# Kernel tuning notes

Hardware: AMD Instinct MI355X
Metric: run time of the kernel (lower is better)

## Reference

```python
import jax, jax.numpy as jnp
import numpy as np

B, S, D, H, HD = 1, 4096, 512, 8, 64
FF = 2048
ROT = 32          # rotary dim (RotaryEmbedding(dim=32))
THETA = 10000.0
EPS = 1e-5


def setup_inputs() -> dict:
    key = jax.random.key(0)
    ks = jax.random.split(key, 10)
    s = 0.02
    return {
        "x": jax.random.normal(ks[0], (B, S, D), jnp.float32),
        "gammas": jnp.ones((2,), jnp.float32),
        "betas": jnp.zeros((2,), jnp.float32),
        "wq": jax.random.normal(ks[1], (D, D), jnp.float32) * s,
        "wk": jax.random.normal(ks[2], (D, D), jnp.float32) * s,
        "wv": jax.random.normal(ks[3], (D, D), jnp.float32) * s,
        "wo": jax.random.normal(ks[4], (D, D), jnp.float32) * s,
        "bo": jnp.zeros((D,), jnp.float32),
        "w1": jax.random.normal(ks[5], (D, FF), jnp.float32) * s,
        "b1": jnp.zeros((FF,), jnp.float32),
        "w2": jax.random.normal(ks[6], (FF, D), jnp.float32) * s,
        "b2": jnp.zeros((D,), jnp.float32),
        "mask": jax.random.randint(ks[7], (B, 1, 1, S), 0, 2, jnp.int32),
    }


def _ln(x):  # LayerNorm, no affine (elementwise_affine=False)
    m = x.mean(-1, keepdims=True)
    v = ((x - m) ** 2).mean(-1, keepdims=True)
    return (x - m) / jnp.sqrt(v + EPS)


def _rope_tables(seq_len, dtype):
    inv_freq = 1.0 / (THETA ** (jnp.arange(0, ROT, 2, dtype=jnp.float32) / ROT))
    freqs = jnp.arange(seq_len, dtype=jnp.float32)[:, None] * inv_freq[None, :]  # (S, ROT/2)
    freqs = jnp.repeat(freqs, 2, axis=-1)  # interleaved: f0,f0,f1,f1,... (S, ROT)
    return jnp.cos(freqs).astype(dtype), jnp.sin(freqs).astype(dtype)


def _apply_rope(t, cos, sin):
    # t: (B,H,S,HD); rotate first ROT dims with interleaved pairs (lucidrains)
    tr, tp = t[..., :ROT], t[..., ROT:]
    x1, x2 = tr[..., 0::2], tr[..., 1::2]
    rot = jnp.stack((-x2, x1), axis=-1).reshape(tr.shape)
    return jnp.concatenate([tr * cos + rot * sin, tp], axis=-1)


def reference(x, gammas, betas, wq, wk, wv, wo, bo, w1, b1, w2, b2, mask):
    # --- attention block ---
    res = x
    h = _ln(x)
    h = gammas[0] * h + betas[0]  # FiLM
    q = (h @ wq).reshape(B, S, H, HD).transpose(0, 2, 1, 3)
    k = (h @ wk).reshape(B, S, H, HD).transpose(0, 2, 1, 3)
    v = (h @ wv).reshape(B, S, H, HD).transpose(0, 2, 1, 3)
    cos, sin = _rope_tables(S, x.dtype)
    q = _apply_rope(q, cos, sin)
    k = _apply_rope(k, cos, sin)
    score = jnp.einsum("bhqd,bhkd->bhqk", q, k) / jnp.sqrt(jnp.asarray(HD, x.dtype))
    score = jnp.where(mask == 0, jnp.asarray(-1e9, x.dtype), score)
    attn = jax.nn.softmax(score, axis=-1)
    out = jnp.einsum("bhqk,bhkd->bhqd", attn, v)
    out = out.transpose(0, 2, 1, 3).reshape(B, S, D)
    x = res + (out @ wo + bo)
    # --- FFN block ---
    res = x
    h = _ln(x)
    h = gammas[1] * h + betas[1]
    h = jax.nn.gelu(h @ w1 + b1, approximate=False) @ w2 + b2
    return res + h
```

## Files before the change

kernel.cpp:

```cpp
#include <hip/hip_runtime.h>
#include <math.h>

constexpr int SEQ  = 4096;
constexpr int DIM  = 512;
constexpr int NH   = 8;
constexpr int HDIM = 64;
constexpr int FFD  = 2048;
constexpr int KSPLIT = 3;

typedef unsigned short u16;
typedef __attribute__((ext_vector_type(8))) short bf16x8;
typedef __attribute__((ext_vector_type(4))) float f32x4;
typedef __attribute__((ext_vector_type(8))) unsigned short u16x8;

#define LOG2E      1.4426950408889634f
#define QSCALE     (0.125f * LOG2E)
#define MASK_OFF   (-1.4427e9f)

static __device__ __forceinline__ u16 f2bf(float x) {
    union { float f; unsigned int u; } v; v.f = x;
    unsigned int r = v.u + 0x7fff + ((v.u >> 16) & 1);
    return (u16)(r >> 16);
}
static __device__ __forceinline__ float bf2f(u16 h) {
    union { unsigned int u; float f; } v; v.u = ((unsigned int)h) << 16;
    return v.f;
}
static __device__ __forceinline__ unsigned int cvtpk(float lo, float hi) {
    unsigned int r;
    asm volatile("v_cvt_pk_bf16_f32 %0, %1, %2" : "=v"(r) : "v"(lo), "v"(hi));
    return r;
}
static __device__ __forceinline__ float exp2f_fast(float x) {
    float r; asm volatile("v_exp_f32 %0, %1" : "=v"(r) : "v"(x)); return r;
}
static __device__ __forceinline__ void gload_lds16(const void* g, void* l) {
    __builtin_amdgcn_global_load_lds(
        (const __attribute__((address_space(1))) unsigned int*)g,
        (__attribute__((address_space(3))) unsigned int*)l, 16, 0, 0);
}

__global__ void prep_kernel(const float* __restrict__ x, u16* __restrict__ h1,
                            const float* __restrict__ gammas, const float* __restrict__ betas,
                            const float* __restrict__ wq, const float* __restrict__ wk,
                            const float* __restrict__ wv, const float* __restrict__ wo,
                            const float* __restrict__ w1, const float* __restrict__ w2,
                            u16* __restrict__ wqkvT, u16* __restrict__ woT,
                            u16* __restrict__ w1T, u16* __restrict__ w2T,
                            const int* __restrict__ mask, float* __restrict__ maskc,
                            int* __restrict__ invidx, int* __restrict__ nkp,
                            float* __restrict__ ct, float* __restrict__ st) {
    __shared__ float smem[1056];
    int b = blockIdx.x;
    int t = threadIdx.x;
    if (b < SEQ / 4) {
        int wv_ = t >> 6, lane = t & 63;
        int row = b * 4 + wv_;
        const float* xr = x + (size_t)row * DIM + lane * 8;
        float4 a0 = *(const float4*)xr;
        float4 a1 = *(const float4*)(xr + 4);
        float f[8] = {a0.x, a0.y, a0.z, a0.w, a1.x, a1.y, a1.z, a1.w};
        float s = 0.f, qs = 0.f;
#pragma unroll
        for (int i = 0; i < 8; i++) { s += f[i]; qs += f[i] * f[i]; }
#pragma unroll
        for (int o = 1; o < 64; o <<= 1) {
            s  += __shfl_xor(s, o, 64);
            qs += __shfl_xor(qs, o, 64);
        }
        float mean = s / DIM;
        float var  = qs / DIM - mean * mean;
        float rstd = rsqrtf(var + 1e-5f);
        float g = gammas[0], be = betas[0];
        u16x8 res;
#pragma unroll
        for (int i = 0; i < 8; i += 2) {
            unsigned int pk = cvtpk(g * ((f[i] - mean) * rstd) + be,
                                    g * ((f[i + 1] - mean) * rstd) + be);
            res[i]     = (u16)(pk & 0xffff);
            res[i + 1] = (u16)(pk >> 16);
        }
        *(u16x8*)(h1 + (size_t)row * DIM + lane * 8) = res;
        return;
    }
    b -= SEQ / 4;
    if (b < 1) {
        __shared__ int cnt[256];
        int base = t * 16;
        int loc[16]; int c = 0;
#pragma unroll
        for (int i = 0; i < 16; i++) { loc[i] = mask[base + i]; c += (loc[i] != 0); }
        cnt[t] = c;
        __syncthreads();
        for (int o = 1; o < 256; o <<= 1) {
            int v = (t >= o) ? cnt[t - o] : 0;
            __syncthreads();
            cnt[t] += v;
            __syncthreads();
        }
        int pos = cnt[t] - c;
        int total = cnt[255];
#pragma unroll
        for (int i = 0; i < 16; i++)
            invidx[base + i] = loc[i] ? pos++ : -1;
#pragma unroll
        for (int i = 0; i < 16; i++)
            maskc[base + i] = (base + i < total) ? 0.0f : MASK_OFF;
        if (t == 0) *nkp = total;
        return;
    }
    b -= 1;
    if (b < 256) {
        int idx = b * 256 + t;
        int s = idx >> 4, i = idx & 15;
        float invf = expf(-(float)i * (9.2103403719761836f / 16.0f));
        float freq = (float)s * invf;
        ct[idx] = cosf(freq);
        st[idx] = sinf(freq);
        return;
    }
    b -= 256;
    const float* src; u16* dst; int K, N; float scale = 1.f;
    if (b < 256)       { src = wq; dst = wqkvT;            K = 512;  N = 512; scale = QSCALE; }
    else if (b < 512)  { src = wk; dst = wqkvT + 512*512;  K = 512;  N = 512; b -= 256; }
    else if (b < 768)  { src = wv; dst = wqkvT + 1024*512; K = 512;  N = 512; b -= 512; }
    else if (b < 1024) { src = wo; dst = woT;              K = 512;  N = 512; b -= 768; }
    else if (b < 2048) { src = w1; dst = w1T;              K = 512;  N = 2048; b -= 1024; }
    else               { src = w2; dst = w2T;              K = 2048; N = 512;  b -= 2048; }
    float (*tile)[33] = (float(*)[33])smem;
    int tiles_x = N / 32;
    int n0 = (b % tiles_x) * 32, k0 = (b / tiles_x) * 32;
    int tx = t & 31, ty = t >> 5;
#pragma unroll
    for (int i = 0; i < 4; i++) {
        int kk = ty + i * 8;
        tile[kk][tx] = src[(size_t)(k0 + kk) * N + n0 + tx];
    }
    __syncthreads();
#pragma unroll
    for (int i = 0; i < 4; i++) {
        int nn = ty + i * 8;
        dst[(size_t)(n0 + nn) * K + k0 + tx] = f2bf(scale * tile[tx][nn]);
    }
}

__global__ void ln_bf16_kernel(const u16* __restrict__ x, u16* __restrict__ out,
                               const float* __restrict__ gammas, const float* __restrict__ betas,
                               int gi) {
    int t = threadIdx.x;
    int wv_ = t >> 6, lane = t & 63;
    int row = blockIdx.x * 4 + wv_;
    u16x8 v = *(const u16x8*)(x + (size_t)row * DIM + lane * 8);
    float f[8];
    float s = 0.f, qs = 0.f;
#pragma unroll
    for (int i = 0; i < 8; i++) { f[i] = bf2f(v[i]); s += f[i]; qs += f[i] * f[i]; }
#pragma unroll
    for (int o = 1; o < 64; o <<= 1) {
        s  += __shfl_xor(s, o, 64);
        qs += __shfl_xor(qs, o, 64);
    }
    float mean = s / DIM;
    float var  = qs / DIM - mean * mean;
    float rstd = rsqrtf(var + 1e-5f);
    float g = gammas[gi], be = betas[gi];
    u16x8 res;
#pragma unroll
    for (int i = 0; i < 8; i += 2) {
        unsigned int pk = cvtpk(g * ((f[i] - mean) * rstd) + be,
                                g * ((f[i + 1] - mean) * rstd) + be);
        res[i]     = (u16)(pk & 0xffff);
        res[i + 1] = (u16)(pk >> 16);
    }
    *(u16x8*)(out + (size_t)row * DIM + lane * 8) = res;
}

constexpr int FLAG_BF16 = 1, FLAG_GELU = 2, FLAG_SPLIT = 4, FLAG_ROPE = 8, FLAG_RESID_BF16 = 16;

template<int MF>
__global__ __launch_bounds__(256) void gemm_bf16(
    const u16* __restrict__ A, const u16* __restrict__ WT,
    const float* __restrict__ bias, const void* __restrict__ resid,
    void* __restrict__ Cq, int M, int N, int K, int flags)
{
    constexpr int BM = MF * 64;
    __shared__ __align__(16) u16 At[2][BM * 128];
    __shared__ __align__(16) u16 Bt[2][64 * 128];
    const int t = threadIdx.x, lane = t & 63, w = t >> 6;
    const int n0 = blockIdx.x * 64, m0 = blockIdx.y * BM;
    const int l15 = lane & 15, l4 = lane >> 4;

    f32x4 acc[MF][4];
#pragma unroll
    for (int m = 0; m < MF; m++)
#pragma unroll
        for (int n = 0; n < 4; n++) acc[m][n] = (f32x4){0.f, 0.f, 0.f, 0.f};

    auto stage = [&](int buf, int k0) {
#pragma unroll
        for (int i = 0; i < MF * 4; i++) {
            int c = (w * MF * 4 + i) * 64 + lane;
            int r = c >> 4, jj = (c & 15) ^ (r & 7);
            gload_lds16(A + (size_t)(m0 + r) * K + k0 + jj * 8,
                        (char*)At[buf] + (w * MF * 4 + i) * 1024);
        }
#pragma unroll
        for (int i = 0; i < 4; i++) {
            int c = (w * 4 + i) * 64 + lane;
            int r = c >> 4, jj = (c & 15) ^ (r & 7);
            gload_lds16(WT + (size_t)(n0 + r) * K + k0 + jj * 8,
                        (char*)Bt[buf] + (w * 4 + i) * 1024);
        }
    };

    const int NT = K / 128;
    stage(0, 0);
    for (int ti = 0; ti < NT; ti++) {
        const int cur = ti & 1;
        asm volatile("s_waitcnt vmcnt(0)" ::: "memory");
        __syncthreads();
        if (ti + 1 < NT) stage(cur ^ 1, (ti + 1) * 128);
        __builtin_amdgcn_s_setprio(1);
#pragma unroll
        for (int kk = 0; kk < 4; kk++) {
            bf16x8 af[MF], bfr[4];
#pragma unroll
            for (int m = 0; m < MF; m++) {
                int row = w * MF * 16 + m * 16 + l15;
                af[m] = *(bf16x8*)((char*)At[cur] + row * 256 +
                                   ((kk * 64 + l4 * 16) ^ ((row & 7) << 4)));
            }
#pragma unroll
            for (int n = 0; n < 4; n++) {
                int row = n * 16 + l15;
                bfr[n] = *(bf16x8*)((char*)Bt[cur] + row * 256 +
                                    ((kk * 64 + l4 * 16) ^ ((row & 7) << 4)));
            }
#pragma unroll
            for (int m = 0; m < MF; m++)
#pragma unroll
                for (int n = 0; n < 4; n++)
                    acc[m][n] = __builtin_amdgcn_mfma_f32_16x16x32_bf16(
                        af[m], bfr[n], acc[m][n], 0, 0, 0);
        }
        __builtin_amdgcn_s_setprio(0);
    }

#pragma unroll
    for (int m = 0; m < MF; m++)
#pragma unroll
        for (int rr = 0; rr < 4; rr++) {
            int row = m0 + w * MF * 16 + m * 16 + l4 * 4 + rr;
#pragma unroll
            for (int n = 0; n < 4; n++) {
                int colg = n0 + n * 16 + l15;
                float cv = acc[m][n][rr];
                if (bias) cv += bias[colg];
                if (flags & FLAG_GELU) cv = 0.5f * cv * (1.0f + erff(cv * 0.70710678118f));
                if (resid) {
                    if (flags & FLAG_RESID_BF16)
                        cv += bf2f(((const u16*)resid)[(size_t)row * N + colg]);
                    else
                        cv += ((const float*)resid)[(size_t)row * N + colg];
                }
                if (flags & FLAG_BF16) {
                    ((u16*)Cq)[(size_t)row * N + colg] = f2bf(cv);
                } else {
                    ((float*)Cq)[(size_t)row * N + colg] = cv;
                }
            }
        }
}

__global__ __launch_bounds__(256) void gemm128(
    const u16* __restrict__ A, const u16* __restrict__ WT,
    const float* __restrict__ bias,
    void* __restrict__ Cq, void* __restrict__ Ck, void* __restrict__ Cv,
    const float* __restrict__ ct, const float* __restrict__ st,
    const int* __restrict__ invidx,
    int M, int N, int K, int flags)
{
    __shared__ __align__(16) u16 At[2][128 * 64];
    __shared__ __align__(16) u16 Bt[2][128 * 64];
    const int t = threadIdx.x, lane = t & 63, w = t >> 6;
    const int wm = w >> 1, wn = w & 1;
    const int n0 = blockIdx.x * 128, m0 = blockIdx.y * 128;
    const int l15 = lane & 15, l4 = lane >> 4;

    f32x4 acc[4][4];
#pragma unroll
    for (int m = 0; m < 4; m++)
#pragma unroll
        for (int n = 0; n < 4; n++) acc[m][n] = (f32x4){0.f, 0.f, 0.f, 0.f};

    auto stage = [&](int buf, int k0) {
#pragma unroll
        for (int i = 0; i < 4; i++) {
            int c = (w * 4 + i) * 64 + lane;
            int r = c >> 3, j = (c & 7) ^ (r & 7);
            gload_lds16(A + (size_t)(m0 + r) * K + k0 + j * 8,
                        (char*)At[buf] + (w * 4 + i) * 1024);
            gload_lds16(WT + (size_t)(n0 + r) * K + k0 + j * 8,
                        (char*)Bt[buf] + (w * 4 + i) * 1024);
        }
    };

    const int NT = K / 64;
    stage(0, 0);
    for (int ti = 0; ti < NT; ti++) {
        const int cur = ti & 1;
        asm volatile("s_waitcnt vmcnt(0)" ::: "memory");
        __syncthreads();
        if (ti + 1 < NT) stage(cur ^ 1, (ti + 1) * 64);
        __builtin_amdgcn_s_setprio(1);
#pragma unroll
        for (int kk = 0; kk < 2; kk++) {
            bf16x8 af[4], bfr[4];
#pragma unroll
            for (int m = 0; m < 4; m++) {
                int row = wm * 64 + m * 16 + l15;
                af[m] = *(bf16x8*)((char*)At[cur] + row * 128 +
                                   ((kk * 64 + l4 * 16) ^ ((row & 7) << 4)));
            }
#pragma unroll
            for (int n = 0; n < 4; n++) {
                int row = wn * 64 + n * 16 + l15;
                bfr[n] = *(bf16x8*)((char*)Bt[cur] + row * 128 +
                                    ((kk * 64 + l4 * 16) ^ ((row & 7) << 4)));
            }
#pragma unroll
            for (int m = 0; m < 4; m++)
#pragma unroll
                for (int n = 0; n < 4; n++)
                    acc[m][n] = __builtin_amdgcn_mfma_f32_16x16x32_bf16(
                        af[m], bfr[n], acc[m][n], 0, 0, 0);
        }
        __builtin_amdgcn_s_setprio(0);
    }

    const int which = (n0 + wn * 64) >> 9;
#pragma unroll
    for (int m = 0; m < 4; m++)
#pragma unroll
        for (int rr = 0; rr < 4; rr++) {
            int row = m0 + wm * 64 + m * 16 + l4 * 4 + rr;
            int orow = row;
            if ((flags & FLAG_SPLIT) && which > 0) orow = invidx[row];
#pragma unroll
            for (int n = 0; n < 4; n++) {
                int colg = n0 + wn * 64 + n * 16 + l15;
                float cv = acc[m][n][rr];
                if (bias) cv += bias[colg];
                if ((flags & FLAG_ROPE) && which < 2 && n < 2) {
                    float partner = __shfl_xor(cv, 1, 64);
                    int i = (n * 16 + l15) >> 1;
                    float cc = ct[row * 16 + i], ss = st[row * 16 + i];
                    cv = (l15 & 1) ? (cv * cc + partner * ss) : (cv * cc - partner * ss);
                }
                if (flags & FLAG_GELU) cv = 0.5f * cv * (1.0f + erff(cv * 0.70710678118f));
                if (flags & FLAG_SPLIT) {
                    if (orow >= 0) {
                        u16* dst = which == 0 ? (u16*)Cq : which == 1 ? (u16*)Ck : (u16*)Cv;
                        dst[(size_t)orow * 512 + (colg & 511)] = f2bf(cv);
                    }
                } else {
                    ((u16*)Cq)[(size_t)row * N + colg] = f2bf(cv);
                }
            }
        }
}

__global__ void transpose_c(const u16* __restrict__ vc, const int* __restrict__ nkp,
                            u16* __restrict__ vTc) {
    int nk = *nkp;
    int s0 = blockIdx.x * 64;
    if (s0 >= ((nk + 63) & ~63)) return;
    __shared__ __align__(16) u16 tile[64][80];
    int h = blockIdx.y;
    int t = threadIdx.x;
#pragma unroll
    for (int p = 0; p < 2; p++) {
        int c = p * 256 + t;
        int r = c >> 3, j = c & 7;
        u16x8 vv = {};
        if (s0 + r < nk)
            vv = *(const u16x8*)(vc + (size_t)(s0 + r) * DIM + h * HDIM + j * 8);
        *(u16x8*)&tile[r][j * 8] = vv;
    }
    __syncthreads();
#pragma unroll
    for (int p = 0; p < 2; p++) {
        int c = p * 256 + t;
        int d = c >> 3, j = c & 7;
        u16x8 vv;
#pragma unroll
        for (int i = 0; i < 8; i++) vv[i] = tile[j * 8 + i][d];
        *(u16x8*)(vTc + ((size_t)h * HDIM + d) * SEQ + s0 + j * 8) = vv;
    }
}

__global__ __launch_bounds__(256, 3) void fattn_kernel(
    const u16* __restrict__ q, const u16* __restrict__ k,
    const u16* __restrict__ vT, const float* __restrict__ maskc,
    const int* __restrict__ nkp,
    u16* __restrict__ Opart, float* __restrict__ lpart)
{
    __shared__ __align__(16) u16 k_s[2][64 * 64];
    __shared__ __align__(16) u16 vt_s[2][64 * 64];
    __shared__ __align__(16) u16 p_s[4][32 * 64];

    const int t = threadIdx.x;
    const int lane = t & 63;
    const int w = t >> 6;
    const int h = blockIdx.x;
    const int q0 = blockIdx.y * 128;
    const int split = blockIdx.z;
    const int nk = *nkp;
    const int ntiles = (nk + 63) >> 6;
    const int tstart = (split * ntiles) / 3;
    const int tend   = ((split + 1) * ntiles) / 3;
    const int l15 = lane & 15, g = lane >> 4;

    bf16x8 qf[2][2];
#pragma unroll
    for (int qh = 0; qh < 2; qh++) {
        const u16* qrow = q + (size_t)(q0 + w * 32 + qh * 16 + l15) * DIM + h * HDIM;
        qf[qh][0] = *(const bf16x8*)(qrow + g * 8);
        qf[qh][1] = *(const bf16x8*)(qrow + g * 8 + 32);
    }

    const bf16x8 ones = (bf16x8){16256, 16256, 16256, 16256, 16256, 16256, 16256, 16256};

    f32x4 O[2][4];
    f32x4 lacc[2];
#pragma unroll
    for (int qh = 0; qh < 2; qh++) {
#pragma unroll
        for (int dt = 0; dt < 4; dt++) O[qh][dt] = (f32x4){0.f, 0.f, 0.f, 0.f};
        lacc[qh] = (f32x4){0.f, 0.f, 0.f, 0.f};
    }

    char* pbase = (char*)p_s[w];
    const int psw = (l15 & 7) << 4;

    auto stage = [&](int buf, int kb2) {
#pragma unroll
        for (int i = 0; i < 2; i++) {
            int c = (w * 2 + i) * 64 + lane;
            int r = c >> 3, j = (c & 7) ^ (r & 7);
            gload_lds16(k + (size_t)(kb2 + r) * DIM + h * HDIM + j * 8,
                        (char*)k_s + buf * 8192 + (w * 2 + i) * 1024);
            gload_lds16(vT + ((size_t)h * HDIM + r) * SEQ + kb2 + j * 8,
                        (char*)vt_s + buf * 8192 + (w * 2 + i) * 1024);
        }
    };

    if (tstart < tend) stage(0, tstart * 64);
    for (int ti = tstart; ti < tend; ti++) {
        const int cur = (ti - tstart) & 1;
        const int kb = ti * 64;
        asm volatile("s_waitcnt vmcnt(0)" ::: "memory");
        __syncthreads();
        if (ti + 1 < tend) stage(cur ^ 1, kb + 64);

        char* kcur = (char*)k_s + cur * 8192;
        char* vcur = (char*)vt_s + cur * 8192;

        f32x4 sacc[2][4];
        __builtin_amdgcn_s_setprio(1);
#pragma unroll
        for (int kt = 0; kt < 4; kt++) {
            int key = kt * 16 + l15;
            int ksw = (key & 7) << 4;
            char* kbase = kcur + key * 128;
            bf16x8 a0 = *(bf16x8*)(kbase + ((g * 16)      ^ ksw));
            bf16x8 a1 = *(bf16x8*)(kbase + ((g * 16 + 64) ^ ksw));
#pragma unroll
            for (int qh = 0; qh < 2; qh++) {
                f32x4 z = (f32x4){0.f, 0.f, 0.f, 0.f};
                z = __builtin_amdgcn_mfma_f32_16x16x32_bf16(a0, qf[qh][0], z, 0, 0, 0);
                z = __builtin_amdgcn_mfma_f32_16x16x32_bf16(a1, qf[qh][1], z, 0, 0, 0);
                sacc[qh][kt] = z;
            }
        }
        __builtin_amdgcn_s_setprio(0);

        const bool haspad = (ti == ntiles - 1);
        if (!haspad) {
#pragma unroll
            for (int qh = 0; qh < 2; qh++)
#pragma unroll
                for (int kt = 0; kt < 4; kt++) {
                    float p0 = exp2f_fast(sacc[qh][kt][0]);
                    float p1 = exp2f_fast(sacc[qh][kt][1]);
                    float p2 = exp2f_fast(sacc[qh][kt][2]);
                    float p3 = exp2f_fast(sacc[qh][kt][3]);
                    uint2 pk;
                    pk.x = cvtpk(p0, p1);
                    pk.y = cvtpk(p2, p3);
                    int colb = (kt * 16 + g * 4) * 2;
                    *(uint2*)(pbase + (qh * 16 + l15) * 128 + (colb ^ psw)) = pk;
                }
        } else {
            float4 mf4[4];
#pragma unroll
            for (int kt = 0; kt < 4; kt++)
                mf4[kt] = *(const float4*)(maskc + kb + kt * 16 + g * 4);
#pragma unroll
            for (int qh = 0; qh < 2; qh++)
#pragma unroll
                for (int kt = 0; kt < 4; kt++) {
                    float p0 = exp2f_fast(sacc[qh][kt][0] + mf4[kt].x);
                    float p1 = exp2f_fast(sacc[qh][kt][1] + mf4[kt].y);
                    float p2 = exp2f_fast(sacc[qh][kt][2] + mf4[kt].z);
                    float p3 = exp2f_fast(sacc[qh][kt][3] + mf4[kt].w);
                    uint2 pk;
                    pk.x = cvtpk(p0, p1);
                    pk.y = cvtpk(p2, p3);
                    int colb = (kt * 16 + g * 4) * 2;
                    *(uint2*)(pbase + (qh * 16 + l15) * 128 + (colb ^ psw)) = pk;
                }
        }

        __builtin_amdgcn_s_setprio(1);
#pragma unroll
        for (int h2 = 0; h2 < 2; h2++) {
            bf16x8 pb[2];
#pragma unroll
            for (int qh = 0; qh < 2; qh++)
                pb[qh] = *(bf16x8*)(pbase + (qh * 16 + l15) * 128 +
                                    (((h2 * 4 + g) * 16) ^ psw));
#pragma unroll
            for (int dt = 0; dt < 4; dt++) {
                int d = dt * 16 + l15;
                bf16x8 va = *(bf16x8*)(vcur + d * 128 +
                                       (((h2 * 4 + g) * 16) ^ ((d & 7) << 4)));
#pragma unroll
                for (int qh = 0; qh < 2; qh++)
                    O[qh][dt] = __builtin_amdgcn_mfma_f32_16x16x32_bf16(
                        va, pb[qh], O[qh][dt], 0, 0, 0);
            }
#pragma unroll
            for (int qh = 0; qh < 2; qh++)
                lacc[qh] = __builtin_amdgcn_mfma_f32_16x16x32_bf16(
                    ones, pb[qh], lacc[qh], 0, 0, 0);
        }
        __builtin_amdgcn_s_setprio(0);
    }

#pragma unroll
    for (int qh = 0; qh < 2; qh++) {
        float lrun = lacc[qh][0];
        int row = q0 + w * 32 + qh * 16 + l15;
        u16* orow = Opart + (size_t)split * SEQ * DIM + (size_t)row * DIM + h * HDIM;
#pragma unroll
        for (int dt = 0; dt < 4; dt++)
#pragma unroll
            for (int r = 0; r < 4; r += 2) {
                unsigned int pk = cvtpk(O[qh][dt][r], O[qh][dt][r + 1]);
                *(unsigned int*)(orow + dt * 16 + 4 * g + r) = pk;
            }
        if (g == 0)
            lpart[((size_t)split * NH + h) * SEQ + row] = lrun;
    }
}

__global__ void attn_combine(const u16* __restrict__ Opart, const float* __restrict__ lpart,
                             u16* __restrict__ out) {
    int t = threadIdx.x;
    int row = blockIdx.x * 4 + (t >> 6);
    int col = (t & 63) * 8;
    int h = col >> 6;
    float l = lpart[(size_t)h * SEQ + row]
            + lpart[((size_t)NH + h) * SEQ + row]
            + lpart[((size_t)2 * NH + h) * SEQ + row];
    float inv = 1.0f / l;
    const size_t SD = (size_t)SEQ * DIM;
    const u16* base = Opart + (size_t)row * DIM + col;
    u16x8 ua = *(const u16x8*)(base);
    u16x8 ub = *(const u16x8*)(base + SD);
    u16x8 uc = *(const u16x8*)(base + 2 * SD);
    u16x8 res;
#pragma unroll
    for (int j = 0; j < 8; j += 2) {
        float o0 = bf2f(ua[j])     + bf2f(ub[j])     + bf2f(uc[j]);
        float o1 = bf2f(ua[j + 1]) + bf2f(ub[j + 1]) + bf2f(uc[j + 1]);
        unsigned int pk = cvtpk(o0 * inv, o1 * inv);
        res[j]     = (u16)(pk & 0xffff);
        res[j + 1] = (u16)(pk >> 16);
    }
    *(u16x8*)(out + (size_t)row * DIM + col) = res;
}

extern "C" void kernel_launch(void* const* d_in, const int* in_sizes, int n_in,
                              void* d_out, int out_size, void* d_ws, size_t ws_size,
                              hipStream_t stream) {
    const float* x      = (const float*)d_in[0];
    const float* gammas = (const float*)d_in[1];
    const float* betas  = (const float*)d_in[2];
    const float* wq     = (const float*)d_in[3];
    const float* wk     = (const float*)d_in[4];
    const float* wv     = (const float*)d_in[5];
    const float* wo     = (const float*)d_in[6];
    const float* bo     = (const float*)d_in[7];
    const float* w1     = (const float*)d_in[8];
    const float* b1     = (const float*)d_in[9];
    const float* w2     = (const float*)d_in[10];
    const float* b2     = (const float*)d_in[11];
    const int*   mask   = (const int*)d_in[12];
    float* out = (float*)d_out;

    char* wsb = (char*)d_ws;
    u16*   h1b   = (u16*)(wsb + 0);
    u16*   kc    = (u16*)(wsb + (4ull  << 20));
    u16*   vc    = (u16*)(wsb + (8ull  << 20));
    u16*   vTc   = (u16*)(wsb + (12ull << 20));
    u16*   qb    = (u16*)(wsb + (16ull << 20));
    u16*   Opart = (u16*)(wsb + (20ull << 20));
    u16*   x2b   = (u16*)(wsb + (20ull << 20));
    u16*   wqkvT = (u16*)(wsb + (32ull << 20));
    u16*   woT   = wqkvT + 1536 * 512;
    u16*   w1T   = woT   + 512 * 512;
    u16*   w2T   = w1T   + 2048 * 512;
    float* maskc = (float*)(wsb + (38ull << 20));
    int*   invidx= (int*)(wsb + (38ull << 20) + (64 << 10));
    int*   nkp   = (int*)(wsb + (38ull << 20) + (128 << 10));
    float* ct    = (float*)(wsb + (39ull << 20));
    float* st    = ct + 65536;
    float* lpart = (float*)(wsb + (40ull << 20));
    u16*   f1b   = h1b;
    u16*   h2b   = qb;
    u16*   attnb = h1b;

    prep_kernel<<<SEQ / 4 + 1 + 256 + 3072, 256, 0, stream>>>(
        x, h1b, gammas, betas, wq, wk, wv, wo, w1, w2,
        wqkvT, woT, w1T, w2T, mask, maskc, invidx, nkp, ct, st);
    gemm128<<<dim3(1536 / 128, SEQ / 128), 256, 0, stream>>>(
        h1b, wqkvT, nullptr, qb, kc, vc, ct, st, invidx,
        SEQ, 1536, DIM, FLAG_SPLIT | FLAG_BF16 | FLAG_ROPE);
    transpose_c<<<dim3(SEQ / 64, NH), 256, 0, stream>>>(vc, nkp, vTc);
    fattn_kernel<<<dim3(NH, SEQ / 128, KSPLIT), 256, 0, stream>>>(
        qb, kc, vTc, maskc, nkp, Opart, lpart);
    attn_combine<<<SEQ / 4, 256, 0, stream>>>(Opart, lpart, attnb);
    gemm_bf16<1><<<dim3(DIM / 64, SEQ / 64), 256, 0, stream>>>(
        attnb, woT, bo, (const void*)x, x2b, SEQ, DIM, DIM, FLAG_BF16);
    ln_bf16_kernel<<<SEQ / 4, 256, 0, stream>>>(x2b, h2b, gammas, betas, 1);
    gemm128<<<dim3(FFD / 128, SEQ / 128), 256, 0, stream>>>(
        h2b, w1T, b1, f1b, nullptr, nullptr, nullptr, nullptr, nullptr,
        SEQ, FFD, DIM, FLAG_BF16 | FLAG_GELU);
    gemm_bf16<1><<<dim3(DIM / 64, SEQ / 64), 256, 0, stream>>>(
        f1b, w2T, b2, (const void*)x2b, out, SEQ, DIM, FFD, FLAG_RESID_BF16);
}
```

Measured before the change: 149.4 us.

## Fuse split-K attention combine into flash-attention kernel via last-block atomic counter

Removes the separate attn_combine launch. Each flash-attention block now takes a per-(head, query-tile) atomic ticket after a threadfence, and the last of the three splits reads the partial outputs and row sums and writes the normalized bf16 attention output. The counters are zeroed in the existing prep kernel. This saves a kernel launch and the gap between kernels, at the cost of extra fences, an atomic per block, and serialized combine work inside the tail blocks.

New measurement: 267.7 us. +79.1%, slower.

```diff
diff --git a/kernel.cpp b/kernel.cpp
--- a/kernel.cpp
+++ b/kernel.cpp
@@ -49,6 +49,7 @@
                             u16* __restrict__ w1T, u16* __restrict__ w2T,
                             const int* __restrict__ mask, float* __restrict__ maskc,
                             int* __restrict__ invidx, int* __restrict__ nkp,
+                            int* __restrict__ ccnt,
                             float* __restrict__ ct, float* __restrict__ st) {
     __shared__ float smem[1056];
     int b = blockIdx.x;
@@ -86,6 +87,7 @@
     b -= SEQ / 4;
     if (b < 1) {
         __shared__ int cnt[256];
+        ccnt[t] = 0;
         int base = t * 16;
         int loc[16]; int c = 0;
 #pragma unroll
@@ -403,7 +405,8 @@
     const u16* __restrict__ q, const u16* __restrict__ k,
     const u16* __restrict__ vT, const float* __restrict__ maskc,
     const int* __restrict__ nkp,
-    u16* __restrict__ Opart, float* __restrict__ lpart)
+    u16* __restrict__ Opart, float* __restrict__ lpart,
+    int* __restrict__ ccnt, u16* __restrict__ attnb)
 {
     __shared__ __align__(16) u16 k_s[2][64 * 64];
     __shared__ __align__(16) u16 vt_s[2][64 * 64];
@@ -563,33 +566,43 @@
         if (g == 0)
             lpart[((size_t)split * NH + h) * SEQ + row] = lrun;
     }
-}
-
-__global__ void attn_combine(const u16* __restrict__ Opart, const float* __restrict__ lpart,
-                             u16* __restrict__ out) {
-    int t = threadIdx.x;
-    int row = blockIdx.x * 4 + (t >> 6);
-    int col = (t & 63) * 8;
-    int h = col >> 6;
-    float l = lpart[(size_t)h * SEQ + row]
-            + lpart[((size_t)NH + h) * SEQ + row]
-            + lpart[((size_t)2 * NH + h) * SEQ + row];
-    float inv = 1.0f / l;
-    const size_t SD = (size_t)SEQ * DIM;
-    const u16* base = Opart + (size_t)row * DIM + col;
-    u16x8 ua = *(const u16x8*)(base);
-    u16x8 ub = *(const u16x8*)(base + SD);
-    u16x8 uc = *(const u16x8*)(base + 2 * SD);
-    u16x8 res;
-#pragma unroll
-    for (int j = 0; j < 8; j += 2) {
-        float o0 = bf2f(ua[j])     + bf2f(ub[j])     + bf2f(uc[j]);
-        float o1 = bf2f(ua[j + 1]) + bf2f(ub[j + 1]) + bf2f(uc[j + 1]);
-        unsigned int pk = cvtpk(o0 * inv, o1 * inv);
-        res[j]     = (u16)(pk & 0xffff);
-        res[j + 1] = (u16)(pk >> 16);
-    }
-    *(u16x8*)(out + (size_t)row * DIM + col) = res;
+
+    __threadfence();
+    __syncthreads();
+    __shared__ int lastFlag;
+    if (t == 0) {
+        int prev = atomicAdd(&ccnt[h * (SEQ / 128) + blockIdx.y], 1);
+        lastFlag = (prev == KSPLIT - 1);
+    }
+    __syncthreads();
+    if (!lastFlag) return;
+    __threadfence();
+    {
+        int row = q0 + (t >> 1);
+        int col = h * HDIM + (t & 1) * 32;
+        float l = lpart[((size_t)0 * NH + h) * SEQ + row]
+                + lpart[((size_t)1 * NH + h) * SEQ + row]
+                + lpart[((size_t)2 * NH + h) * SEQ + row];
+        float inv = 1.0f / l;
+        const size_t SD = (size_t)SEQ * DIM;
+        const u16* base = Opart + (size_t)row * DIM + col;
+#pragma unroll
+        for (int chunk = 0; chunk < 4; chunk++) {
+            u16x8 ua = *(const u16x8*)(base + chunk * 8);
+            u16x8 ub = *(const u16x8*)(base + SD + chunk * 8);
+            u16x8 uc = *(const u16x8*)(base + 2 * SD + chunk * 8);
+            u16x8 res;
+#pragma unroll
+            for (int j = 0; j < 8; j += 2) {
+                float o0 = bf2f(ua[j])     + bf2f(ub[j])     + bf2f(uc[j]);
+                float o1 = bf2f(ua[j + 1]) + bf2f(ub[j + 1]) + bf2f(uc[j + 1]);
+                unsigned int pk = cvtpk(o0 * inv, o1 * inv);
+                res[j]     = (u16)(pk & 0xffff);
+                res[j + 1] = (u16)(pk >> 16);
+            }
+            *(u16x8*)(attnb + (size_t)row * DIM + col + chunk * 8) = res;
+        }
+    }
 }
 
 extern "C" void kernel_launch(void* const* d_in, const int* in_sizes, int n_in,
@@ -628,20 +641,20 @@
     float* ct    = (float*)(wsb + (39ull << 20));
     float* st    = ct + 65536;
     float* lpart = (float*)(wsb + (40ull << 20));
+    int*   ccnt  = (int*)(wsb + (40ull << 20) + (512 << 10));
     u16*   f1b   = h1b;
     u16*   h2b   = qb;
     u16*   attnb = h1b;
 
     prep_kernel<<<SEQ / 4 + 1 + 256 + 3072, 256, 0, stream>>>(
         x, h1b, gammas, betas, wq, wk, wv, wo, w1, w2,
-        wqkvT, woT, w1T, w2T, mask, maskc, invidx, nkp, ct, st);
+        wqkvT, woT, w1T, w2T, mask, maskc, invidx, nkp, ccnt, ct, st);
     gemm128<<<dim3(1536 / 128, SEQ / 128), 256, 0, stream>>>(
         h1b, wqkvT, nullptr, qb, kc, vc, ct, st, invidx,
         SEQ, 1536, DIM, FLAG_SPLIT | FLAG_BF16 | FLAG_ROPE);
     transpose_c<<<dim3(SEQ / 64, NH), 256, 0, stream>>>(vc, nkp, vTc);
     fattn_kernel<<<dim3(NH, SEQ / 128, KSPLIT), 256, 0, stream>>>(
-        qb, kc, vTc, maskc, nkp, Opart, lpart);
-    attn_combine<<<SEQ / 4, 256, 0, stream>>>(Opart, lpart, attnb);
+        qb, kc, vTc, maskc, nkp, Opart, lpart, ccnt, attnb);
     gemm_bf16<1><<<dim3(DIM / 64, SEQ / 64), 256, 0, stream>>>(
         attnb, woT, bo, (const void*)x, x2b, SEQ, DIM, DIM, FLAG_BF16);
     ln_bf16_kernel<<<SEQ / 4, 256, 0, stream>>>(x2b, h2b, gammas, betas, 1);
```
